# Optimization experiments

Hardware: AMD Instinct MI355X
Metric: run time of the kernel (lower is better)

The kernel has to match this reference:

```python
import jax, jax.numpy as jnp
import numpy as np

B, T, C = 2, 2048, 1024
NH, HD = 16, 64  # n_head, head_dim (qk == vo)


def setup_inputs() -> dict:
    key = jax.random.key(0)
    ks = jax.random.split(key, 5)
    scale = 1.0 / np.sqrt(C)
    return {
        "x": jax.random.normal(ks[0], (B, T, C), dtype=jnp.float32),
        "Wq": jax.random.normal(ks[1], (C, C), dtype=jnp.float32) * scale,
        "Wk": jax.random.normal(ks[2], (C, C), dtype=jnp.float32) * scale,
        "Wv": jax.random.normal(ks[3], (C, C), dtype=jnp.float32) * scale,
        "Wo": jax.random.normal(ks[4], (C, C), dtype=jnp.float32) * scale,
    }


def reference(x, Wq, Wk, Wv, Wo):
    # torch Linear: y = x @ W.T (weights stored [out, in])
    q = (x @ Wq.T).reshape(B, T, NH, HD).transpose(0, 2, 1, 3)  # [B,H,T,D]
    k = (x @ Wk.T).reshape(B, T, NH, HD).transpose(0, 2, 1, 3)
    v = (x @ Wv.T).reshape(B, T, NH, HD).transpose(0, 2, 1, 3)
    att = jnp.einsum("bhqd,bhkd->bhqk", q, k) * (1.0 / np.sqrt(HD))
    causal = jnp.tril(jnp.ones((T, T), dtype=bool))
    att = jnp.where(causal[None, None], att, -jnp.inf)
    att = jax.nn.softmax(att, axis=-1)
    y = jnp.einsum("bhqk,bhkd->bhqd", att, v)  # [B,H,T,D]
    y = y.transpose(0, 2, 1, 3).reshape(B, T, NH * HD)
    return y @ Wo.T  # dropout p=0 -> identity
```

## Files before the change

kernel.cpp:

```cpp
#include <hip/hip_runtime.h>
#include <hip/hip_bf16.h>
#include <cstdint>
#include <cstddef>
#include <cmath>

#define B_  2
#define T_  2048
#define C_  1024
#define NH_ 16
#define HD_ 64

typedef __bf16 bf16;
typedef bf16  bf16x8 __attribute__((ext_vector_type(8)));
typedef bf16  bf16x4 __attribute__((ext_vector_type(4)));
typedef float f32x4  __attribute__((ext_vector_type(4)));
typedef float f32x16 __attribute__((ext_vector_type(16)));

#define MFMA16(a, b, c) __builtin_amdgcn_mfma_f32_16x16x32_bf16((a), (b), (c), 0, 0, 0)
#define MFMA32(a, b, c) __builtin_amdgcn_mfma_f32_32x32x16_bf16((a), (b), (c), 0, 0, 0)

__device__ __forceinline__ void gld_lds16(const bf16* g, bf16* lds_base_uniform) {
    __builtin_amdgcn_global_load_lds(
        (const __attribute__((address_space(1))) uint32_t*)g,
        (__attribute__((address_space(3))) uint32_t*)lds_base_uniform,
        16, 0, 0);
}

__global__ __launch_bounds__(256) void cast_all(const float* __restrict__ x,
                                                const float* __restrict__ Wq,
                                                const float* __restrict__ Wk,
                                                const float* __restrict__ Wv,
                                                const float* __restrict__ Wo,
                                                bf16* __restrict__ xb,
                                                bf16* __restrict__ Wqk,
                                                bf16* __restrict__ Wvb,
                                                bf16* __restrict__ Wob) {
    const int bid = blockIdx.x;
    if (bid < 4096) {
        const int i = bid * 256 + threadIdx.x;
        float4 v = ((const float4*)x)[i];
        ((bf16x4*)xb)[i] = bf16x4{ (bf16)v.x, (bf16)v.y, (bf16)v.z, (bf16)v.w };
    } else {
        const float C1 = 0.1803368801111f;
        const int i = (bid - 4096) * 256 + threadIdx.x;
        const int nw4 = C_ * C_ / 4;
        float4 q = ((const float4*)Wq)[i];
        float4 k = ((const float4*)Wk)[i];
        float4 v = ((const float4*)Wv)[i];
        float4 o = ((const float4*)Wo)[i];
        ((bf16x4*)Wqk)[i]       = bf16x4{ (bf16)(q.x * C1), (bf16)(q.y * C1),
                                          (bf16)(q.z * C1), (bf16)(q.w * C1) };
        ((bf16x4*)Wqk)[nw4 + i] = bf16x4{ (bf16)k.x, (bf16)k.y, (bf16)k.z, (bf16)k.w };
        ((bf16x4*)Wvb)[i]       = bf16x4{ (bf16)v.x, (bf16)v.y, (bf16)v.z, (bf16)v.w };
        ((bf16x4*)Wob)[i]       = bf16x4{ (bf16)o.x, (bf16)o.y, (bf16)o.z, (bf16)o.w };
    }
}

__device__ __forceinline__ void gemm_tile(bf16* As, bf16* Bs,
                                          const bf16* __restrict__ A,
                                          const bf16* __restrict__ W,
                                          bf16* __restrict__ Y,
                                          int N, int K, int m0, int n0) {
    const int tid  = threadIdx.x;
    const int lane = tid & 63;
    const int w    = tid >> 6;
    const int ml   = lane & 15;
    const int quad = lane >> 4;
    const int wm   = (w >> 1) * 64;
    const int wn   = (w & 1) * 64;
    const int sr   = lane >> 2;
    const int sc   = lane & 3;

    f32x4 acc[4][4] = {};

    auto stage = [&](int k0, int buf) {
#pragma unroll
        for (int ei = 0; ei < 2; ++ei) {
            const int e = w * 2 + ei;
            gld_lds16(A + (size_t)(m0 + e * 16 + sr) * K + k0 + sc * 8, &As[buf * 4096 + e * 512]);
            gld_lds16(W + (size_t)(n0 + e * 16 + sr) * K + k0 + sc * 8, &Bs[buf * 4096 + e * 512]);
        }
    };

    stage(0, 0);
    __builtin_amdgcn_s_waitcnt(0);
    __syncthreads();

    int buf = 0;
    for (int k0 = 0; k0 < K; k0 += 32, buf ^= 1) {
        if (k0 + 32 < K) stage(k0 + 32, buf ^ 1);

        bf16x8 af[4], bfr[4];
#pragma unroll
        for (int t = 0; t < 4; ++t) {
            af[t]  = *(const bf16x8*)&As[buf * 4096 + (wm + t * 16 + ml) * 32 + quad * 8];
            bfr[t] = *(const bf16x8*)&Bs[buf * 4096 + (wn + t * 16 + ml) * 32 + quad * 8];
        }
#pragma unroll
        for (int mt = 0; mt < 4; ++mt)
#pragma unroll
            for (int nt = 0; nt < 4; ++nt)
                acc[mt][nt] = MFMA16(af[mt], bfr[nt], acc[mt][nt]);

        if (k0 + 32 < K) {
            __builtin_amdgcn_s_waitcnt(0);
            __syncthreads();
        }
    }

#pragma unroll
    for (int mt = 0; mt < 4; ++mt)
#pragma unroll
        for (int nt = 0; nt < 4; ++nt)
#pragma unroll
            for (int r = 0; r < 4; ++r) {
                const int row = m0 + wm + mt * 16 + quad * 4 + r;
                const int col = n0 + wn + nt * 16 + ml;
                Y[(size_t)row * N + col] = (bf16)acc[mt][nt][r];
            }
}

__global__ __launch_bounds__(256) void proj_fused(const bf16* __restrict__ xb,
                                                  const bf16* __restrict__ Wqk,
                                                  const bf16* __restrict__ Wvb,
                                                  bf16* __restrict__ QKb,
                                                  bf16* __restrict__ VtT) {
    __shared__ __align__(16) bf16 As[2][128 * 32];
    __shared__ __align__(16) bf16 Bs[2][128 * 32];
    const int bid = blockIdx.x;
    if (bid < 512) {
        gemm_tile(&As[0][0], &Bs[0][0], xb, Wqk, QKb, 2048, 1024, (bid >> 4) * 128, (bid & 15) * 128);
    } else {
        const int b2 = bid - 512;
        gemm_tile(&As[0][0], &Bs[0][0], Wvb, xb, VtT, 4096, 1024, (b2 >> 5) * 128, (b2 & 31) * 128);
    }
}

__global__ __launch_bounds__(256) void gemm_wo(const bf16* __restrict__ A,
                                               const bf16* __restrict__ W,
                                               float* __restrict__ Y) {
    __shared__ __align__(16) bf16 As[2][64 * 32];
    __shared__ __align__(16) bf16 Bs[2][128 * 32];
    const int tid  = threadIdx.x;
    const int lane = tid & 63;
    const int w    = tid >> 6;
    const int ml   = lane & 15;
    const int quad = lane >> 4;
    const int wm   = (w >> 1) * 32;
    const int wn   = (w & 1) * 64;
    const int m0   = blockIdx.y * 64;
    const int n0   = blockIdx.x * 128;
    const int sr   = lane >> 2;
    const int sc   = lane & 3;

    f32x4 acc[2][4] = {};

    auto stage = [&](int k0, int buf) {
        gld_lds16(A + (size_t)(m0 + w * 16 + sr) * 1024 + k0 + sc * 8, &As[buf][w * 512]);
#pragma unroll
        for (int ei = 0; ei < 2; ++ei) {
            const int e = w * 2 + ei;
            gld_lds16(W + (size_t)(n0 + e * 16 + sr) * 1024 + k0 + sc * 8, &Bs[buf][e * 512]);
        }
    };

    stage(0, 0);
    __builtin_amdgcn_s_waitcnt(0);
    __syncthreads();

    int buf = 0;
    for (int k0 = 0; k0 < 1024; k0 += 32, buf ^= 1) {
        if (k0 + 32 < 1024) stage(k0 + 32, buf ^ 1);

        bf16x8 af[2], bfr[4];
#pragma unroll
        for (int t = 0; t < 2; ++t)
            af[t] = *(const bf16x8*)&As[buf][(wm + t * 16 + ml) * 32 + quad * 8];
#pragma unroll
        for (int t = 0; t < 4; ++t)
            bfr[t] = *(const bf16x8*)&Bs[buf][(wn + t * 16 + ml) * 32 + quad * 8];
#pragma unroll
        for (int mt = 0; mt < 2; ++mt)
#pragma unroll
            for (int nt = 0; nt < 4; ++nt)
                acc[mt][nt] = MFMA16(af[mt], bfr[nt], acc[mt][nt]);

        if (k0 + 32 < 1024) {
            __builtin_amdgcn_s_waitcnt(0);
            __syncthreads();
        }
    }

#pragma unroll
    for (int mt = 0; mt < 2; ++mt)
#pragma unroll
        for (int nt = 0; nt < 4; ++nt)
#pragma unroll
            for (int r = 0; r < 4; ++r) {
                const int row = m0 + wm + mt * 16 + quad * 4 + r;
                const int col = n0 + wn + nt * 16 + ml;
                Y[(size_t)row * 1024 + col] = acc[mt][nt][r];
            }
}

__global__ __launch_bounds__(256, 4) void attn_mfma(const bf16* __restrict__ QKb,
                                                    const bf16* __restrict__ VtT,
                                                    bf16* __restrict__ Pbuf,
                                                    float* __restrict__ Lbuf) {
    const int bid = blockIdx.x;
    const int hb  = bid & 31;
    const int s   = 39 - (bid >> 5);
    int it, chunk;
    if (s < 4)       { it = s;                  chunk = 0; }
    else if (s < 12) { it = 4 + ((s - 4) >> 1); chunk = (s - 4) & 1; }
    else if (s < 24) { it = 8 + (s - 12) / 3;   chunk = (s - 12) % 3; }
    else             { it = 12 + ((s - 24) >> 2); chunk = (s - 24) & 3; }
    const int h = hb >> 1, b = hb & 1;

    const int tid  = threadIdx.x;
    const int lane = tid & 63;
    const int w    = tid >> 6;
    const int keyl = lane & 31;
    const int hi   = lane >> 5;

    __shared__ __align__(16) bf16 Ks[2][4096];
    __shared__ __align__(16) bf16 Vs[2][4096];

    const bf16* Qbase = QKb + (size_t)b * T_ * 2048 + (size_t)h * HD_;
    const bf16* Kbase = Qbase + 1024;
    const bf16* Vbase = VtT + (size_t)h * HD_ * 4096 + (size_t)b * T_;

    const int qrow = it * 128 + w * 32 + keyl;
    bf16x8 qf[4];
#pragma unroll
    for (int dc = 0; dc < 4; ++dc)
        qf[dc] = *(const bf16x8*)(Qbase + (size_t)qrow * 2048 + dc * 16 + hi * 8);

    f32x16 o_acc[2] = {};
    float l_run = 0.f;

    const int ktbase  = chunk * 8;
    const int nrounds = min(8, 2 * it + 2 - ktbase);

    auto stageKV = [&](int ktg, int buf) {
        const int k0 = ktg * 64;
#pragma unroll
        for (int ei = 0; ei < 2; ++ei) {
            const int e  = w * 2 + ei;
            const int rr = e * 8 + (lane >> 3);
            const int g  = (lane & 7) ^ (lane >> 3);
            gld_lds16(Kbase + (size_t)(k0 + rr) * 2048 + g * 8, &Ks[buf][e * 512]);
            gld_lds16(Vbase + (size_t)rr * 4096 + k0 + g * 8, &Vs[buf][e * 512]);
        }
    };

    auto round = [&](int cur, int ktg) {
        const int k0 = ktg * 64;
        const bool domask = (k0 + 63) > (it * 128 + w * 32);
        const int qg = it * 128 + w * 32 + keyl;
#pragma unroll
        for (int kh = 0; kh < 2; ++kh) {
            f32x16 sacc = {};
#pragma unroll
            for (int dc = 0; dc < 4; ++dc) {
                bf16x8 kf = *(const bf16x8*)&Ks[cur][(kh * 32 + keyl) * 64 +
                                                     (((dc << 1) | hi) ^ (keyl & 7)) * 8];
                sacc = MFMA32(kf, qf[dc], sacc);
            }
#pragma unroll
            for (int c = 0; c < 2; ++c) {
                float p[8];
#pragma unroll
                for (int r8 = 0; r8 < 8; ++r8) {
                    float arg = sacc[8 * c + r8];
                    if (domask) {
                        const int kg = k0 + kh * 32 + 16 * c + 8 * (r8 >> 2) + 4 * hi + (r8 & 3);
                        if (kg > qg) arg = -1e30f;
                    }
                    p[r8] = __builtin_amdgcn_exp2f(arg);
                }
                l_run += ((p[0] + p[1]) + (p[2] + p[3])) + ((p[4] + p[5]) + (p[6] + p[7]));
                uint32_t a0, a1, b0, b1;
                asm("v_cvt_pk_bf16_f32 %0, %1, %2" : "=v"(a0) : "v"(p[0]), "v"(p[1]));
                asm("v_cvt_pk_bf16_f32 %0, %1, %2" : "=v"(a1) : "v"(p[2]), "v"(p[3]));
                asm("v_cvt_pk_bf16_f32 %0, %1, %2" : "=v"(b0) : "v"(p[4]), "v"(p[5]));
                asm("v_cvt_pk_bf16_f32 %0, %1, %2" : "=v"(b1) : "v"(p[6]), "v"(p[7]));
                asm("v_permlane32_swap_b32 %0, %1" : "+v"(a0), "+v"(b0));
                asm("v_permlane32_swap_b32 %0, %1" : "+v"(a1), "+v"(b1));
                union { uint32_t d[4]; bf16x8 v; } pa;
                pa.d[0] = a0; pa.d[1] = a1; pa.d[2] = b0; pa.d[3] = b1;
                const int kc = 2 * kh + c;
#pragma unroll
                for (int dh = 0; dh < 2; ++dh) {
                    bf16x8 vf = *(const bf16x8*)&Vs[cur][(dh * 32 + keyl) * 64 +
                                                         (((kc << 1) | hi) ^ (keyl & 7)) * 8];
                    o_acc[dh] = MFMA32(pa.v, vf, o_acc[dh]);
                }
            }
        }
    };

    stageKV(ktbase, 0);
    asm volatile("s_waitcnt vmcnt(0)" ::: "memory");
    asm volatile("s_barrier" ::: "memory");

    for (int j = 0; j < nrounds; ++j) {
        const int cur = j & 1;
        const int ktg = ktbase + j;
        if (j + 1 < nrounds) stageKV(ktg + 1, cur ^ 1);
        round(cur, ktg);
        if (j + 1 < nrounds) {
            asm volatile("s_waitcnt vmcnt(0)" ::: "memory");
            asm volatile("s_barrier" ::: "memory");
        }
    }

    const int slotIdx = hb * 40 + s;
    bf16* pb = Pbuf + (size_t)slotIdx * 8192;
#pragma unroll
    for (int dh = 0; dh < 2; ++dh)
#pragma unroll
        for (int r = 0; r < 16; ++r) {
            const int qloc = w * 32 + (r & 3) + 8 * (r >> 2) + 4 * hi;
            pb[qloc * 64 + dh * 32 + keyl] = (bf16)o_acc[dh][r];
        }
    const float l_tot = l_run + __shfl_xor(l_run, 32);
    if (hi == 0)
        Lbuf[slotIdx * 128 + w * 32 + keyl] = l_tot;
}

__global__ __launch_bounds__(256) void attn_merge(const bf16* __restrict__ Pbuf,
                                                  const float* __restrict__ Lbuf,
                                                  bf16* __restrict__ Ab) {
    const int gid = blockIdx.x;
    const int it  = gid >> 5;
    const int hb  = gid & 31;
    const int h = hb >> 1, b = hb & 1;
    int s0;
    if (it < 4)       s0 = it;
    else if (it < 8)  s0 = 4 + (it - 4) * 2;
    else if (it < 12) s0 = 12 + (it - 8) * 3;
    else              s0 = 24 + (it - 12) * 4;
    const int nch = (2 * it + 9) >> 3;

    const int tid = threadIdx.x;
    const int row = tid >> 1;
    const int cg  = (tid & 1) * 32;

    float acc[32] = {};
    float lsum = 0.f;
    for (int c = 0; c < nch; ++c) {
        const int slot = hb * 40 + s0 + c;
        lsum += Lbuf[slot * 128 + row];
        const bf16* pb = Pbuf + (size_t)slot * 8192 + row * 64 + cg;
#pragma unroll
        for (int g = 0; g < 4; ++g) {
            bf16x8 v = *(const bf16x8*)(pb + g * 8);
#pragma unroll
            for (int j = 0; j < 8; ++j) acc[g * 8 + j] += (float)v[j];
        }
    }
    const float rcl = 1.0f / lsum;
    bf16* dst = Ab + (size_t)(b * T_ + it * 128 + row) * 1024 + h * 64 + cg;
#pragma unroll
    for (int g = 0; g < 4; ++g) {
        bf16x8 o;
#pragma unroll
        for (int j = 0; j < 8; ++j) o[j] = (bf16)(acc[g * 8 + j] * rcl);
        *(bf16x8*)(dst + g * 8) = o;
    }
}

extern "C" void kernel_launch(void* const* d_in, const int* in_sizes, int n_in,
                              void* d_out, int out_size, void* d_ws, size_t ws_size,
                              hipStream_t stream) {
    const float* x  = (const float*)d_in[0];
    const float* Wq = (const float*)d_in[1];
    const float* Wk = (const float*)d_in[2];
    const float* Wv = (const float*)d_in[3];
    const float* Wo = (const float*)d_in[4];
    float* out = (float*)d_out;

    const size_t n_x = (size_t)B_ * T_ * C_;
    const size_t n_w = (size_t)C_ * C_;

    bf16* xb   = (bf16*)d_ws;
    bf16* Wqk  = xb + n_x;
    bf16* Wvb  = Wqk + 2 * n_w;
    bf16* Wob  = Wvb + n_w;
    bf16* QKb  = Wob + n_w;
    bf16* VtT  = QKb + 2 * n_x;
    bf16* Ab   = VtT + n_x;
    bf16* Pbuf = Ab + n_x;
    float* Lbuf = (float*)(Pbuf + (size_t)1280 * 8192);

    cast_all<<<5120, 256, 0, stream>>>(x, Wq, Wk, Wv, Wo, xb, Wqk, Wvb, Wob);

    proj_fused<<<768, 256, 0, stream>>>(xb, Wqk, Wvb, QKb, VtT);

    attn_mfma<<<1280, 256, 0, stream>>>(QKb, VtT, Pbuf, Lbuf);
    attn_merge<<<512, 256, 0, stream>>>(Pbuf, Lbuf, Ab);

    gemm_wo<<<dim3(1024 / 128, 4096 / 64), 256, 0, stream>>>(Ab, Wob, out);
}
```

Before: 177.9 us.

## Triple-buffer GEMM LDS staging with partial vmcnt waits to prefetch two tiles ahead

Both projection GEMMs (the fused QKV tile and the Wo GEMM) move from double to triple LDS buffering. Loads are now issued two k-steps ahead, and each iteration waits only for the older stage through a partial vmcnt count instead of draining every outstanding load. This is meant to hide global-load latency behind the MFMA work. In exchange it uses 1.5x the LDS per block, which may reduce occupancy, and it depends on the hand-picked vmcnt values matching the number of loads issued per stage.

```diff
diff --git a/kernel.cpp b/kernel.cpp
--- a/kernel.cpp
+++ b/kernel.cpp
@@ -83,12 +83,16 @@
     };
 
     stage(0, 0);
-    __builtin_amdgcn_s_waitcnt(0);
-    __syncthreads();
+    stage(32, 1);
+    asm volatile("s_waitcnt vmcnt(4)" ::: "memory");
+    __builtin_amdgcn_s_barrier();
 
     int buf = 0;
-    for (int k0 = 0; k0 < K; k0 += 32, buf ^= 1) {
-        if (k0 + 32 < K) stage(k0 + 32, buf ^ 1);
+    for (int k0 = 0; k0 < K; k0 += 32) {
+        const int bnext = (buf == 2) ? 0 : buf + 1;
+        const int bpre  = (bnext == 2) ? 0 : bnext + 1;
+        const int kpre  = k0 + 64;
+        if (kpre < K) stage(kpre, bpre);
 
         bf16x8 af[4], bfr[4];
 #pragma unroll
@@ -103,9 +107,11 @@
                 acc[mt][nt] = MFMA16(af[mt], bfr[nt], acc[mt][nt]);
 
         if (k0 + 32 < K) {
-            __builtin_amdgcn_s_waitcnt(0);
-            __syncthreads();
-        }
+            if (kpre < K) { asm volatile("s_waitcnt vmcnt(4)" ::: "memory"); }
+            else          { asm volatile("s_waitcnt vmcnt(0)" ::: "memory"); }
+            __builtin_amdgcn_s_barrier();
+        }
+        buf = bnext;
     }
 
 #pragma unroll
@@ -125,8 +131,8 @@
                                                   const bf16* __restrict__ Wvb,
                                                   bf16* __restrict__ QKb,
                                                   bf16* __restrict__ VtT) {
-    __shared__ __align__(16) bf16 As[2][128 * 32];
-    __shared__ __align__(16) bf16 Bs[2][128 * 32];
+    __shared__ __align__(16) bf16 As[3][128 * 32];
+    __shared__ __align__(16) bf16 Bs[3][128 * 32];
     const int bid = blockIdx.x;
     if (bid < 512) {
         gemm_tile(&As[0][0], &Bs[0][0], xb, Wqk, QKb, 2048, 1024, (bid >> 4) * 128, (bid & 15) * 128);
@@ -139,8 +145,8 @@
 __global__ __launch_bounds__(256) void gemm_wo(const bf16* __restrict__ A,
                                                const bf16* __restrict__ W,
                                                float* __restrict__ Y) {
-    __shared__ __align__(16) bf16 As[2][64 * 32];
-    __shared__ __align__(16) bf16 Bs[2][128 * 32];
+    __shared__ __align__(16) bf16 As[3][64 * 32];
+    __shared__ __align__(16) bf16 Bs[3][128 * 32];
     const int tid  = threadIdx.x;
     const int lane = tid & 63;
     const int w    = tid >> 6;
@@ -165,12 +171,16 @@
     };
 
     stage(0, 0);
-    __builtin_amdgcn_s_waitcnt(0);
-    __syncthreads();
+    stage(32, 1);
+    asm volatile("s_waitcnt vmcnt(3)" ::: "memory");
+    __builtin_amdgcn_s_barrier();
 
     int buf = 0;
-    for (int k0 = 0; k0 < 1024; k0 += 32, buf ^= 1) {
-        if (k0 + 32 < 1024) stage(k0 + 32, buf ^ 1);
+    for (int k0 = 0; k0 < 1024; k0 += 32) {
+        const int bnext = (buf == 2) ? 0 : buf + 1;
+        const int bpre  = (bnext == 2) ? 0 : bnext + 1;
+        const int kpre  = k0 + 64;
+        if (kpre < 1024) stage(kpre, bpre);
 
         bf16x8 af[2], bfr[4];
 #pragma unroll
@@ -186,9 +196,11 @@
                 acc[mt][nt] = MFMA16(af[mt], bfr[nt], acc[mt][nt]);
 
         if (k0 + 32 < 1024) {
-            __builtin_amdgcn_s_waitcnt(0);
-            __syncthreads();
-        }
+            if (kpre < 1024) { asm volatile("s_waitcnt vmcnt(3)" ::: "memory"); }
+            else             { asm volatile("s_waitcnt vmcnt(0)" ::: "memory"); }
+            __builtin_amdgcn_s_barrier();
+        }
+        buf = bnext;
     }
 
 #pragma unroll
```

Result: slower. 213.4 us (+20.0%).
